# Kernel tuning notes

Measured on AMD Instinct MI355X. Metric: run time of the kernel, lower is better.

The kernel has to match this reference:

```python
import jax, jax.numpy as jnp
import numpy as np

N = 100000      # nodes per node type (asset, zone)
E = 1000000     # edges per edge type
HID = 64        # hidden_dim
HEADS = 2
CH = HID // HEADS  # 32, GATConv out_channels per head
L = 2           # num_layers
A = 64          # action_count
NG = 6          # global features
FW = 2 * HID + NG  # 134 feature width for heads


def _gat(xs_in, xd_in, W, a_src, a_dst, bias, src, dst, n_dst):
    """PyG GATConv (v1, add_self_loops=False, concat=True) for one edge type.
    xs_in: [Ns, HID] source feats, xd_in: [Nd, HID] dest feats (same lin weight W).
    Returns [n_dst, HEADS*CH]."""
    xs = (xs_in @ W).reshape(-1, HEADS, CH)
    xd = (xd_in @ W).reshape(-1, HEADS, CH)
    al_s = jnp.einsum('nhc,hc->nh', xs, a_src)
    al_d = jnp.einsum('nhc,hc->nh', xd, a_dst)
    al = jax.nn.leaky_relu(al_s[src] + al_d[dst], 0.2)       # [E, H]
    mx = jax.ops.segment_max(al, dst, num_segments=n_dst)    # segment softmax (stable)
    mx = jnp.where(jnp.isfinite(mx), mx, 0.0)                # empty segments
    ex = jnp.exp(al - mx[dst])
    den = jax.ops.segment_sum(ex, dst, num_segments=n_dst)
    w = ex / (den[dst] + 1e-16)                              # PyG softmax eps
    msg = xs[src] * w[:, :, None]                            # [E, H, C]
    out = jax.ops.segment_sum(msg.reshape(msg.shape[0], HEADS * CH), dst, num_segments=n_dst)
    return out + bias


def setup_inputs() -> dict:
    key = jax.random.key(0)
    ks = jax.random.split(key, 24)
    s = 0.05
    inp = {
        'x_asset': jax.random.normal(ks[0], (N, 16), jnp.float32),
        'x_zone': jax.random.normal(ks[1], (N, 32), jnp.float32),
        'ei_zz': jax.random.randint(ks[2], (2, E), 0, N, dtype=jnp.int32),
        'ei_az': jax.random.randint(ks[3], (2, E), 0, N, dtype=jnp.int32),
        'ei_za': jax.random.randint(ks[4], (2, E), 0, N, dtype=jnp.int32),
        'gvec': jax.random.uniform(ks[5], (NG,), jnp.float32),
        'mask': jax.random.randint(ks[6], (A,), 0, 2) == 1,
        'proj_W_asset': jax.random.normal(ks[7], (16, HID), jnp.float32) * s,
        'proj_b_asset': jnp.zeros((HID,), jnp.float32),
        'proj_W_zone': jax.random.normal(ks[8], (32, HID), jnp.float32) * s,
        'proj_b_zone': jnp.zeros((HID,), jnp.float32),
        'gat_W': jax.random.normal(ks[9], (L, 3, HID, HID), jnp.float32) * s,
        'gat_asrc': jax.random.normal(ks[10], (L, 3, HEADS, CH), jnp.float32) * s,
        'gat_adst': jax.random.normal(ks[11], (L, 3, HEADS, CH), jnp.float32) * s,
        'gat_bias': jnp.zeros((L, 3, HID), jnp.float32),
        'actor_W1': jax.random.normal(ks[12], (FW, HID), jnp.float32) * s,
        'actor_b1': jnp.zeros((HID,), jnp.float32),
        'actor_W2': jax.random.normal(ks[13], (HID, A), jnp.float32) * s,
        'actor_b2': jnp.zeros((A,), jnp.float32),
        'critic_W1': jax.random.normal(ks[14], (FW, HID), jnp.float32) * s,
        'critic_b1': jnp.zeros((HID,), jnp.float32),
        'critic_W2': jax.random.normal(ks[15], (HID, 1), jnp.float32) * s,
        'critic_b2': jnp.zeros((1,), jnp.float32),
    }
    return inp


def reference(x_asset, x_zone, ei_zz, ei_az, ei_za, gvec, mask,
              proj_W_asset, proj_b_asset, proj_W_zone, proj_b_zone,
              gat_W, gat_asrc, gat_adst, gat_bias,
              actor_W1, actor_b1, actor_W2, actor_b2,
              critic_W1, critic_b1, critic_W2, critic_b2):
    # input projections per node type
    ha = x_asset @ proj_W_asset + proj_b_asset   # [N, HID]
    hz = x_zone @ proj_W_zone + proj_b_zone      # [N, HID]
    # HeteroConv stack: edge types 0=(zone,near,zone) 1=(asset,in,zone) 2=(zone,contains,asset), aggr='sum'
    for l in range(L):
        z_zz = _gat(hz, hz, gat_W[l, 0], gat_asrc[l, 0], gat_adst[l, 0], gat_bias[l, 0], ei_zz[0], ei_zz[1], N)
        z_az = _gat(ha, hz, gat_W[l, 1], gat_asrc[l, 1], gat_adst[l, 1], gat_bias[l, 1], ei_az[0], ei_az[1], N)
        a_za = _gat(hz, ha, gat_W[l, 2], gat_asrc[l, 2], gat_adst[l, 2], gat_bias[l, 2], ei_za[0], ei_za[1], N)
        hz = jax.nn.relu(z_zz + z_az)
        ha = jax.nn.relu(a_za)
    # mean pool per node type, sorted order: asset, zone
    pooled = jnp.concatenate([ha.mean(axis=0), hz.mean(axis=0)])
    feats = jnp.concatenate([pooled, gvec])      # [FW]
    logits = jax.nn.relu(feats @ actor_W1 + actor_b1) @ actor_W2 + actor_b2   # [A]
    value = jax.nn.relu(feats @ critic_W1 + critic_b1) @ critic_W2 + critic_b2  # [1]
    m = jnp.where(mask.any(), mask, jnp.ones_like(mask))
    masked = jnp.where(m, logits, -jnp.inf)
    return jnp.concatenate([masked, value])      # [A+1]: masked logits + value
```

## Files before the change

kernel.cpp:

```cpp
#include <hip/hip_runtime.h>
#include <math.h>

#define CE 8192
#define BSH 9
#define BMAXB 512
#define ASTR 104
#define DSTR 72

typedef __attribute__((ext_vector_type(8))) short bf16x8;
typedef __attribute__((ext_vector_type(4))) float f32x4;
typedef __attribute__((ext_vector_type(2))) float f32x2;

__device__ __forceinline__ unsigned short f2bf(float f) {
    unsigned u = __float_as_uint(f);
    u += 0x7fffu + ((u >> 16) & 1u);
    return (unsigned short)(u >> 16);
}
__device__ __forceinline__ float bf2f(unsigned short u) {
    return __uint_as_float(((unsigned)u) << 16);
}

__global__ __launch_bounds__(256) void gemm2_k(const float* __restrict__ Xa,
                                               const float* __restrict__ Xz,
                                               const float* __restrict__ Wa,
                                               const float* __restrict__ Wz,
                                               const float* __restrict__ ba,
                                               const float* __restrict__ bz,
                                               unsigned short* __restrict__ outa,
                                               unsigned short* __restrict__ outz,
                                               int n) {
    const int y = blockIdx.y;
    const float* X = y ? Xz : Xa;
    const float* W = y ? Wz : Wa;
    const float* bias = y ? bz : ba;
    unsigned short* outb = y ? outz : outa;
    const int kshift = y ? 5 : 4;
    const int K = 1 << kshift;

    __shared__ float sXt[64 * 68];
    __shared__ float sW[64 * 64];
    __shared__ float sB[64];
    const int tid = threadIdx.x;
    const int row0 = blockIdx.x * 64;

    for (int i = tid * 4; i < 64 * K; i += 1024) {
        int r = i >> kshift, k = i & (K - 1);
        int row = row0 + r;
        float4 v = make_float4(0.f, 0.f, 0.f, 0.f);
        if (row < n) v = *(const float4*)(X + (size_t)row * K + k);
        sXt[(k + 0) * 68 + r] = v.x;
        sXt[(k + 1) * 68 + r] = v.y;
        sXt[(k + 2) * 68 + r] = v.z;
        sXt[(k + 3) * 68 + r] = v.w;
    }
    for (int i = tid * 4; i < K * 64; i += 1024)
        *(float4*)(sW + i) = *(const float4*)(W + i);
    if (tid < 64) sB[tid] = bias[tid];
    __syncthreads();

    const int tc = tid & 15, tr = tid >> 4;
    float acc[4][4] = {};
#pragma unroll 8
    for (int k = 0; k < K; ++k) {
        float4 a = *(const float4*)(sXt + k * 68 + tr * 4);
        float4 b = *(const float4*)(sW + k * 64 + tc * 4);
        acc[0][0] += a.x * b.x; acc[0][1] += a.x * b.y; acc[0][2] += a.x * b.z; acc[0][3] += a.x * b.w;
        acc[1][0] += a.y * b.x; acc[1][1] += a.y * b.y; acc[1][2] += a.y * b.z; acc[1][3] += a.y * b.w;
        acc[2][0] += a.z * b.x; acc[2][1] += a.z * b.y; acc[2][2] += a.z * b.z; acc[2][3] += a.z * b.w;
        acc[3][0] += a.w * b.x; acc[3][1] += a.w * b.y; acc[3][2] += a.w * b.z; acc[3][3] += a.w * b.w;
    }
#pragma unroll
    for (int i = 0; i < 4; ++i) {
        int row = row0 + tr * 4 + i;
        if (row < n) {
            float4 o;
            o.x = acc[i][0] + sB[tc * 4 + 0];
            o.y = acc[i][1] + sB[tc * 4 + 1];
            o.z = acc[i][2] + sB[tc * 4 + 2];
            o.w = acc[i][3] + sB[tc * 4 + 3];
            ushort4 v4 = make_ushort4(f2bf(o.x), f2bf(o.y), f2bf(o.z), f2bf(o.w));
            *(ushort4*)(outb + (size_t)row * 64 + tc * 4) = v4;
        }
    }
}

__global__ void prep_k(const float* __restrict__ gW, const float* __restrict__ gad,
                       unsigned short* __restrict__ Wbt, float* __restrict__ Wd3All) {
    int b = blockIdx.x;
    int t = threadIdx.x;
    if (b < 6) {
        for (int i = t; i < 4096; i += 384) {
            int nn = i >> 6, k = i & 63;
            Wbt[(size_t)b * 4096 + i] = f2bf(gW[(size_t)b * 4096 + k * 64 + nn]);
        }
    } else {
        int l = b - 6;
        int et = t >> 7, r = t & 127;
        int k = r >> 1, h = r & 1;
        const float* W = gW + (size_t)l * 3 * 4096 + et * 4096;
        const float* adst = gad + (size_t)l * 3 * 64 + et * 64;
        float s = 0.f;
        for (int c = 0; c < 32; ++c) s += W[k * 64 + h * 32 + c] * adst[h * 32 + c];
        Wd3All[l * 384 + t] = s;
    }
}

__global__ __launch_bounds__(256) void gemm_mfma3_k(const unsigned short* __restrict__ hzb,
                                                    const unsigned short* __restrict__ hab,
                                                    const unsigned short* __restrict__ WbtL,
                                                    const float* __restrict__ gasL,
                                                    const float* __restrict__ Wd3,
                                                    unsigned char* __restrict__ ts0,
                                                    unsigned char* __restrict__ ts1,
                                                    unsigned char* __restrict__ ts2,
                                                    float2* __restrict__ als0,
                                                    float2* __restrict__ als1,
                                                    float2* __restrict__ als2,
                                                    float2* __restrict__ ald_zz,
                                                    float2* __restrict__ ald_az,
                                                    float2* __restrict__ ald_za, int n) {
    const int et = blockIdx.y;
    const unsigned short* Xb = (et == 1) ? hab : hzb;
    const unsigned short* Wt = WbtL + (size_t)et * 4096;
    const float* asrc = gasL + et * 64;
    unsigned char* ts8 = (et == 0) ? ts0 : (et == 1) ? ts1 : ts2;
    float2* alsOut = (et == 0) ? als0 : (et == 1) ? als1 : als2;

    __shared__ unsigned short sA[64 * ASTR];
    __shared__ unsigned short sB[64 * ASTR];
    __shared__ float sAs[64];
    __shared__ float sWd[384];
    const int tid = threadIdx.x;
    const int row0 = blockIdx.x * 64;

    for (int i = tid; i < 512; i += 256) {
        int r = i >> 3, seg = i & 7;
        int row = row0 + r;
        uint4 v = make_uint4(0, 0, 0, 0);
        if (row < n) v = *(const uint4*)(Xb + (size_t)row * 64 + seg * 8);
        *(uint4*)(sA + r * ASTR + seg * 8) = v;
    }
    for (int i = tid; i < 512; i += 256) {
        int nn = i >> 3, seg = i & 7;
        *(uint4*)(sB + nn * ASTR + seg * 8) = *(const uint4*)(Wt + nn * 64 + seg * 8);
    }
    if (tid < 64) sAs[tid] = asrc[tid];
    for (int i = tid; i < 384; i += 256) sWd[i] = Wd3[i];
    __syncthreads();

    const int lane = tid & 63;
    const int w = tid >> 6;
    const int m = lane & 15, q = lane >> 4;

    bf16x8 a0 = *(const bf16x8*)(sA + (w * 16 + m) * ASTR + q * 8);
    bf16x8 a1 = *(const bf16x8*)(sA + (w * 16 + m) * ASTR + 32 + q * 8);
    f32x4 acc[4];
#pragma unroll
    for (int c = 0; c < 4; ++c) {
        bf16x8 b0 = *(const bf16x8*)(sB + (c * 16 + m) * ASTR + q * 8);
        bf16x8 b1 = *(const bf16x8*)(sB + (c * 16 + m) * ASTR + 32 + q * 8);
        f32x4 z = {0.f, 0.f, 0.f, 0.f};
        z = __builtin_amdgcn_mfma_f32_16x16x32_bf16(a0, b0, z, 0, 0, 0);
        z = __builtin_amdgcn_mfma_f32_16x16x32_bf16(a1, b1, z, 0, 0, 0);
        acc[c] = z;
    }
    float s0[4], s1[4];
#pragma unroll
    for (int r = 0; r < 4; ++r) {
        s0[r] = acc[0][r] * sAs[m] + acc[1][r] * sAs[16 + m];
        s1[r] = acc[2][r] * sAs[32 + m] + acc[3][r] * sAs[48 + m];
    }
#pragma unroll
    for (int off = 1; off < 16; off <<= 1) {
#pragma unroll
        for (int r = 0; r < 4; ++r) { s0[r] += __shfl_xor(s0[r], off); s1[r] += __shfl_xor(s1[r], off); }
    }
    if (m < 4) {
        int row = row0 + w * 16 + q * 4 + m;
        if (row < n) alsOut[row] = make_float2(s0[m], s1[m]);
    }

    if (et != 2) {
        const int rid = tid >> 2, part = tid & 3;
        const int row = row0 + rid;
        const unsigned short* rp = sA + rid * ASTR + part * 16;
        bf16x8 x0 = *(const bf16x8*)rp;
        bf16x8 x1 = *(const bf16x8*)(rp + 8);
        float xv[16];
#pragma unroll
        for (int i = 0; i < 8; ++i) {
            xv[i]     = bf2f((unsigned short)x0[i]);
            xv[8 + i] = bf2f((unsigned short)x1[i]);
        }
        const float* wd = sWd + (et == 0 ? 0 : 256);
        float p0 = 0.f, p1 = 0.f, t0 = 0.f, t1 = 0.f;
#pragma unroll
        for (int i = 0; i < 16; ++i) {
            int k = part * 16 + i;
            p0 += xv[i] * wd[2 * k];
            p1 += xv[i] * wd[2 * k + 1];
        }
        if (et == 0) {
#pragma unroll
            for (int i = 0; i < 16; ++i) {
                int k = part * 16 + i;
                t0 += xv[i] * sWd[128 + 2 * k];
                t1 += xv[i] * sWd[128 + 2 * k + 1];
            }
        }
        p0 += __shfl_xor(p0, 1); p0 += __shfl_xor(p0, 2);
        p1 += __shfl_xor(p1, 1); p1 += __shfl_xor(p1, 2);
        t0 += __shfl_xor(t0, 1); t0 += __shfl_xor(t0, 2);
        t1 += __shfl_xor(t1, 1); t1 += __shfl_xor(t1, 2);
        if (part == 0 && row < n) {
            if (et == 0) {
                ald_zz[row] = make_float2(p0, p1);
                ald_az[row] = make_float2(t0, t1);
            } else {
                ald_za[row] = make_float2(p0, p1);
            }
        }
    }

    __syncthreads();
    unsigned char* sD = (unsigned char*)sA;
#pragma unroll
    for (int c = 0; c < 4; ++c) {
        int pk01 = __builtin_amdgcn_cvt_pk_fp8_f32(acc[c][0], acc[c][1], 0, false);
        int pk23 = __builtin_amdgcn_cvt_pk_fp8_f32(acc[c][2], acc[c][3], 0, false);
        int rb = w * 16 + q * 4;
        int col = c * 16 + m;
        sD[(rb + 0) * DSTR + col] = (unsigned char)(pk01 & 0xff);
        sD[(rb + 1) * DSTR + col] = (unsigned char)((pk01 >> 8) & 0xff);
        sD[(rb + 2) * DSTR + col] = (unsigned char)(pk23 & 0xff);
        sD[(rb + 3) * DSTR + col] = (unsigned char)((pk23 >> 8) & 0xff);
    }
    __syncthreads();
    for (int i = tid; i < 512; i += 256) {
        int r = i >> 3, seg = i & 7;
        int row = row0 + r;
        if (row < n)
            *(uint2*)(ts8 + (size_t)row * 64 + seg * 8) = *(const uint2*)(sD + r * DSTR + seg * 8);
    }
}

__global__ __launch_bounds__(1024) void chunk_hist_k(const int* __restrict__ e0p,
                                                     const int* __restrict__ e1p,
                                                     const int* __restrict__ e2p,
                                                     int* __restrict__ cnt,
                                                     int E, int CB, int NBr) {
    int b = blockIdx.x;
    int et = b / CB, c = b - et * CB;
    const int* dst = (et == 0 ? e0p : et == 1 ? e1p : e2p) + E;
    __shared__ int lcnt[BMAXB];
    int t = threadIdx.x;
    for (int i = t; i < NBr; i += 1024) lcnt[i] = 0;
    __syncthreads();
    int base = c * CE;
    for (int i = t; i < CE; i += 1024) {
        int e = base + i;
        if (e < E) atomicAdd(&lcnt[dst[e] >> BSH], 1);
    }
    __syncthreads();
    int rowbase = et * NBr;
    for (int i = t; i < NBr; i += 1024) cnt[(size_t)(rowbase + i) * CB + c] = lcnt[i];
}
__global__ __launch_bounds__(256) void row_scan_k(int* __restrict__ cnt,
                                                  int* __restrict__ btot, int CB) {
    size_t row = (size_t)blockIdx.x * CB;
    __shared__ int buf[512];
    int t = threadIdx.x;
    int o0 = (t < CB) ? cnt[row + t] : 0;
    int o1 = (t + 256 < CB) ? cnt[row + t + 256] : 0;
    buf[t] = o0; buf[t + 256] = o1;
    __syncthreads();
    for (int off = 1; off < 512; off <<= 1) {
        int v0 = (t >= off) ? buf[t - off] : 0;
        int v1 = (t + 256 >= off) ? buf[t + 256 - off] : 0;
        __syncthreads();
        buf[t] += v0; buf[t + 256] += v1;
        __syncthreads();
    }
    if (t < CB) cnt[row + t] = buf[t] - o0;
    if (t + 256 < CB) cnt[row + t + 256] = buf[t + 256] - o1;
    if (t == 0) btot[blockIdx.x] = buf[511];
}
__global__ __launch_bounds__(1024) void btot_scan_k(const int* __restrict__ btot,
                                                    int* __restrict__ bbase,
                                                    int* __restrict__ bOff,
                                                    int NT, int E,
                                                    int* __restrict__ rowptrAll, int N) {
    __shared__ int buf[1024];
    int t = threadIdx.x;
    int v = (t < NT) ? btot[t] : 0;
    buf[t] = v;
    __syncthreads();
    for (int off = 1; off < 1024; off <<= 1) {
        int u = (t >= off) ? buf[t - off] : 0;
        __syncthreads();
        buf[t] += u;
        __syncthreads();
    }
    if (t < NT) { int e = buf[t] - v; bbase[t] = e; bOff[t] = e; }
    if (t == 0) {
        bOff[NT] = 3 * E;
        rowptrAll[N] = E;
        rowptrAll[(N + 1) + N] = 2 * E;
        rowptrAll[2 * (N + 1) + N] = 3 * E;
    }
}
__global__ __launch_bounds__(1024) void chunk_scatter_k(const int* __restrict__ e0p,
                                                        const int* __restrict__ e1p,
                                                        const int* __restrict__ e2p,
                                                        const int* __restrict__ cnt,
                                                        const int* __restrict__ bbase,
                                                        int* __restrict__ pairs,
                                                        int E, int CB, int NBr) {
    int b = blockIdx.x;
    int et = b / CB, c = b - et * CB;
    const int* eb = (et == 0 ? e0p : et == 1 ? e1p : e2p);
    __shared__ int lcur[BMAXB];
    int t = threadIdx.x;
    int rb = et * NBr;
    for (int i = t; i < NBr; i += 1024) lcur[i] = bbase[rb + i] + cnt[(size_t)(rb + i) * CB + c];
    __syncthreads();
    int base = c * CE;
    for (int i = t; i < CE; i += 1024) {
        int e = base + i;
        if (e < E) {
            int d = eb[E + e];
            int pos = atomicAdd(&lcur[d >> BSH], 1);
            pairs[pos] = ((d & (BMAXB - 1)) << 20) | eb[e];
        }
    }
}
__global__ __launch_bounds__(512) void bucket_local_k(const int* __restrict__ pairs,
                                                      const int* __restrict__ bOff,
                                                      int* __restrict__ rowptrAll,
                                                      int* __restrict__ ssrc, int N, int NBr) {
    int b = blockIdx.x;
    int et = b / NBr, lb = b - et * NBr;
    int beg = bOff[b], end = bOff[b + 1];
    int node0 = lb << BSH;
    int* rowptr = rowptrAll + (size_t)et * (N + 1);
    __shared__ int deg[512];
    __shared__ int cur[512];
    __shared__ int wsum[8];
    int t = threadIdx.x, lane = t & 63, wq = t >> 6;
    deg[t] = 0;
    __syncthreads();
    for (int j = beg + t; j < end; j += 512)
        atomicAdd(&deg[pairs[j] >> 20], 1);
    __syncthreads();
    int v = deg[t];
    int x = v;
#pragma unroll
    for (int off = 1; off < 64; off <<= 1) {
        int u = __shfl_up(x, off);
        if (lane >= off) x += u;
    }
    if (lane == 63) wsum[wq] = x;
    __syncthreads();
    int basep = 0;
#pragma unroll
    for (int q = 0; q < 8; ++q) basep += (q < wq) ? wsum[q] : 0;
    int e0 = beg + basep + x - v;
    cur[t] = e0;
    int n0 = node0 + t;
    if (n0 < N) rowptr[n0] = e0;
    __syncthreads();
    for (int j = beg + t; j < end; j += 512) {
        int p = pairs[j];
        int pos = atomicAdd(&cur[p >> 20], 1);
        ssrc[pos] = p & 0xFFFFF;
    }
}

__global__ __launch_bounds__(256) void gat_out2_k(const int* __restrict__ rowptr0,
                                                  const int* __restrict__ rowptr1,
                                                  const int* __restrict__ rowptr2,
                                                  const int* __restrict__ ssrc,
                                                  const float2* __restrict__ als0,
                                                  const float2* __restrict__ ald0,
                                                  const unsigned char* __restrict__ ts0,
                                                  const float2* __restrict__ als1,
                                                  const float2* __restrict__ ald1,
                                                  const unsigned char* __restrict__ ts1,
                                                  const float2* __restrict__ als2,
                                                  const float2* __restrict__ ald2,
                                                  const unsigned char* __restrict__ ts2,
                                                  const float* __restrict__ gbL,
                                                  unsigned short* __restrict__ outHz,
                                                  unsigned short* __restrict__ outHa,
                                                  int n) {
    const int y = blockIdx.y;
    const int nseg = y ? 1 : 2;
    int lane = threadIdx.x & 63;
    int gl = lane & 15;
    int wid = blockIdx.x * 16 + (threadIdx.x >> 4);
    if (wid >= n) return;
    const int r = gl >> 3;
    const int c0 = (gl & 7) * 8;
    const int gbase = lane & 48;

    float acc8[8] = {};
    for (int seg = 0; seg < nseg; ++seg) {
        const int* rowptr;
        const float2 *als, *ald;
        const unsigned char* ts8;
        if (y) { rowptr = rowptr2; als = als2; ald = ald2; ts8 = ts2; }
        else if (seg == 0) { rowptr = rowptr0; als = als0; ald = ald0; ts8 = ts0; }
        else { rowptr = rowptr1; als = als1; ald = ald1; ts8 = ts1; }
        int beg = rowptr[wid], end = rowptr[wid + 1];
        if (beg == end) continue;
        float2 bd = ald[wid];
        float d0 = 0.f, d1 = 0.f;
        float a8[8] = {};
        for (int cbeg = beg; cbeg < end; cbeg += 16) {
            int j = cbeg + gl;
            int s = 0; float e0 = 0.f, e1 = 0.f;
            if (j < end) {
                s = ssrc[j];
                float2 a = als[s];
                float l0 = a.x + bd.x; l0 = l0 > 0.f ? l0 : 0.2f * l0;
                float l1 = a.y + bd.y; l1 = l1 > 0.f ? l1 : 0.2f * l1;
                e0 = __expf(l0); e1 = __expf(l1);
            }
            d0 += e0; d1 += e1;
            int cnt = min(16, end - cbeg);
            uint2 rr[8]; float wv[8];
#pragma unroll
            for (int k = 0; k < 8; ++k) {
                int jj = 2 * k;
                if (jj < cnt) {
                    int srcLane = gbase + jj + r;
                    int sj = __shfl(s, srcLane);
                    float w0 = __shfl(e0, srcLane), w1 = __shfl(e1, srcLane);
                    float w = (c0 < 32) ? w0 : w1;
                    bool live = (jj + r) < cnt;
                    wv[k] = live ? w : 0.f;
                    if (live) rr[k] = *(const uint2*)(ts8 + (size_t)sj * 64 + c0);
                    else rr[k] = make_uint2(0, 0);
                } else { wv[k] = 0.f; rr[k] = make_uint2(0, 0); }
            }
#pragma unroll
            for (int k = 0; k < 8; ++k) {
                float w = wv[k];
                if (w != 0.f) {
                    f32x2 p0 = __builtin_amdgcn_cvt_pk_f32_fp8(rr[k].x, false);
                    f32x2 p1 = __builtin_amdgcn_cvt_pk_f32_fp8(rr[k].x, true);
                    f32x2 p2 = __builtin_amdgcn_cvt_pk_f32_fp8(rr[k].y, false);
                    f32x2 p3 = __builtin_amdgcn_cvt_pk_f32_fp8(rr[k].y, true);
                    a8[0] += p0.x * w; a8[1] += p0.y * w;
                    a8[2] += p1.x * w; a8[3] += p1.y * w;
                    a8[4] += p2.x * w; a8[5] += p2.y * w;
                    a8[6] += p3.x * w; a8[7] += p3.y * w;
                }
            }
        }
#pragma unroll
        for (int off = 1; off < 16; off <<= 1) { d0 += __shfl_xor(d0, off); d1 += __shfl_xor(d1, off); }
#pragma unroll
        for (int i = 0; i < 8; ++i) a8[i] += __shfl_xor(a8[i], 8);
        float inv = (c0 < 32) ? 1.f / (d0 + 1e-16f) : 1.f / (d1 + 1e-16f);
#pragma unroll
        for (int i = 0; i < 8; ++i) acc8[i] += a8[i] * inv;
    }

    if (r == 0) {
        const float* biasA = y ? gbL + 128 : gbL;
        const float* biasB = y ? nullptr : gbL + 64;
        float4 bA1 = *(const float4*)(biasA + c0);
        float4 bA2 = *(const float4*)(biasA + c0 + 4);
        float b8[8] = { bA1.x, bA1.y, bA1.z, bA1.w, bA2.x, bA2.y, bA2.z, bA2.w };
        if (biasB) {
            float4 bB1 = *(const float4*)(biasB + c0);
            float4 bB2 = *(const float4*)(biasB + c0 + 4);
            b8[0] += bB1.x; b8[1] += bB1.y; b8[2] += bB1.z; b8[3] += bB1.w;
            b8[4] += bB2.x; b8[5] += bB2.y; b8[6] += bB2.z; b8[7] += bB2.w;
        }
        float v8[8];
#pragma unroll
        for (int i = 0; i < 8; ++i) v8[i] = fmaxf(acc8[i] + b8[i], 0.f);
        unsigned short* outBf = y ? outHa : outHz;
        unsigned short* bp = outBf + (size_t)wid * 64 + c0;
        ushort4 u1 = make_ushort4(f2bf(v8[0]), f2bf(v8[1]), f2bf(v8[2]), f2bf(v8[3]));
        ushort4 u2 = make_ushort4(f2bf(v8[4]), f2bf(v8[5]), f2bf(v8[6]), f2bf(v8[7]));
        *(ushort4*)bp = u1;
        *(ushort4*)(bp + 4) = u2;
    }
}

__global__ __launch_bounds__(256) void pool_k(const unsigned short* __restrict__ hab,
                                              const unsigned short* __restrict__ hzb,
                                              float* __restrict__ sums, int n) {
    __shared__ float red[2][16][64];
    int tid = threadIdx.x;
    int c4 = (tid & 15) * 4;
    int rq = tid >> 4;
    float la[4] = {}, lz[4] = {};
    for (int row = blockIdx.x * 16 + rq; row < n; row += gridDim.x * 16) {
        ushort4 va = *(const ushort4*)(hab + (size_t)row * 64 + c4);
        ushort4 vz = *(const ushort4*)(hzb + (size_t)row * 64 + c4);
        la[0] += bf2f(va.x); la[1] += bf2f(va.y); la[2] += bf2f(va.z); la[3] += bf2f(va.w);
        lz[0] += bf2f(vz.x); lz[1] += bf2f(vz.y); lz[2] += bf2f(vz.z); lz[3] += bf2f(vz.w);
    }
#pragma unroll
    for (int i = 0; i < 4; ++i) { red[0][rq][c4 + i] = la[i]; red[1][rq][c4 + i] = lz[i]; }
    __syncthreads();
    if (tid < 64) {
        float ta = 0.f, tz = 0.f;
#pragma unroll
        for (int rr = 0; rr < 16; ++rr) { ta += red[0][rr][tid]; tz += red[1][rr][tid]; }
        atomicAdd(sums + tid, ta);
        atomicAdd(sums + 64 + tid, tz);
    }
}

__global__ __launch_bounds__(64) void head_k(const float* __restrict__ sums,
                                             const float* __restrict__ gvec,
                                             const unsigned char* __restrict__ mask,
                                             const float* __restrict__ aW1, const float* __restrict__ ab1,
                                             const float* __restrict__ aW2, const float* __restrict__ ab2,
                                             const float* __restrict__ cW1, const float* __restrict__ cb1,
                                             const float* __restrict__ cW2, const float* __restrict__ cb2,
                                             float* __restrict__ out, float invn) {
    __shared__ float f[134];
    __shared__ float h1a[64];
    int t = threadIdx.x;
    f[t] = sums[t] * invn;
    f[64 + t] = sums[64 + t] * invn;
    if (t < 6) f[128 + t] = gvec[t];
    __syncthreads();
    float a = ab1[t], c = cb1[t];
    for (int i = 0; i < 134; ++i) {
        float fv = f[i];
        a += fv * aW1[i * 64 + t];
        c += fv * cW1[i * 64 + t];
    }
    h1a[t] = fmaxf(a, 0.f);
    float vp = fmaxf(c, 0.f) * cW2[t];
    __syncthreads();
    float lg = ab2[t];
    for (int j = 0; j < 64; ++j) lg += h1a[j] * aW2[j * 64 + t];
    for (int off = 32; off; off >>= 1) vp += __shfl_down(vp, off);
    unsigned char mb = mask[t];
    unsigned long long bal = __ballot(mb != 0);
    float ov = (bal == 0ull || mb) ? lg : -3.0e38f;
    out[t] = ov;
    if (t == 0) out[64] = vp + cb2[0];
}

extern "C" void kernel_launch(void* const* d_in, const int* in_sizes, int n_in,
                              void* d_out, int out_size, void* d_ws, size_t ws_size,
                              hipStream_t stream) {
    const float* x_asset = (const float*)d_in[0];
    const float* x_zone  = (const float*)d_in[1];
    const int* ei[3] = { (const int*)d_in[2], (const int*)d_in[3], (const int*)d_in[4] };
    const float* gvec = (const float*)d_in[5];
    const unsigned char* mask = (const unsigned char*)d_in[6];
    const float* pWa = (const float*)d_in[7];
    const float* pba = (const float*)d_in[8];
    const float* pWz = (const float*)d_in[9];
    const float* pbz = (const float*)d_in[10];
    const float* gW  = (const float*)d_in[11];
    const float* gas = (const float*)d_in[12];
    const float* gad = (const float*)d_in[13];
    const float* gb  = (const float*)d_in[14];
    const float* aW1 = (const float*)d_in[15];
    const float* ab1 = (const float*)d_in[16];
    const float* aW2 = (const float*)d_in[17];
    const float* ab2 = (const float*)d_in[18];
    const float* cW1 = (const float*)d_in[19];
    const float* cb1 = (const float*)d_in[20];
    const float* cW2 = (const float*)d_in[21];
    const float* cb2 = (const float*)d_in[22];

    const int N = in_sizes[0] / 16;
    const int E = in_sizes[2] / 2;
    const int NBr = (N + 511) >> BSH;
    const int CB  = (E + CE - 1) / CE;
    const int NT  = 3 * NBr;

    float* ws = (float*)d_ws;
    size_t off = 0;
    unsigned short* hab = (unsigned short*)(ws + off); off += (size_t)N * 32;
    unsigned short* hzb = (unsigned short*)(ws + off); off += (size_t)N * 32;
    unsigned char* ts3[3];
    for (int et = 0; et < 3; ++et) { ts3[et] = (unsigned char*)(ws + off); off += (size_t)N * 16; }
    float2* als3[3];
    for (int et = 0; et < 3; ++et) { als3[et] = (float2*)(ws + off); off += (size_t)2 * N; }
    float2* ald3[3];
    for (int et = 0; et < 3; ++et) { ald3[et] = (float2*)(ws + off); off += (size_t)2 * N; }
    unsigned short* Wbt = (unsigned short*)(ws + off); off += 12288 + 64;
    float* Wd3All = ws + off; off += 768;
    float* sums = ws + off; off += 128;
    int* rowptrAll = (int*)(ws + off); off += (size_t)3 * (N + 1);
    int* ssrcAll   = (int*)(ws + off); off += (size_t)3 * E;
    int* pairs     = (int*)(ws + off); off += (size_t)3 * E;
    int* cnt   = (int*)(ws + off); off += (size_t)NT * CB;
    int* btot  = (int*)(ws + off); off += 1024;
    int* bbase = (int*)(ws + off); off += 1024;
    int* bOff  = (int*)(ws + off); off += (size_t)(NT + 1);

    const int gGemm = (N + 63) / 64;
    const int gGat  = (N + 15) / 16;

    chunk_hist_k<<<3 * CB, 1024, 0, stream>>>(ei[0], ei[1], ei[2], cnt, E, CB, NBr);
    row_scan_k<<<NT, 256, 0, stream>>>(cnt, btot, CB);
    btot_scan_k<<<1, 1024, 0, stream>>>(btot, bbase, bOff, NT, E, rowptrAll, N);
    chunk_scatter_k<<<3 * CB, 1024, 0, stream>>>(ei[0], ei[1], ei[2], cnt, bbase, pairs, E, CB, NBr);
    bucket_local_k<<<NT, 512, 0, stream>>>(pairs, bOff, rowptrAll, ssrcAll, N, NBr);

    prep_k<<<8, 384, 0, stream>>>(gW, gad, Wbt, Wd3All);
    gemm2_k<<<dim3(gGemm, 2), 256, 0, stream>>>(x_asset, x_zone, pWa, pWz, pba, pbz,
                                                hab, hzb, N);

    for (int l = 0; l < 2; ++l) {
        gemm_mfma3_k<<<dim3(gGemm, 3), 256, 0, stream>>>(hzb, hab,
                                                         Wbt + (size_t)l * 3 * 4096,
                                                         gas + (size_t)l * 3 * 64,
                                                         Wd3All + (size_t)l * 384,
                                                         ts3[0], ts3[1], ts3[2],
                                                         als3[0], als3[1], als3[2],
                                                         ald3[0], ald3[1], ald3[2], N);
        gat_out2_k<<<dim3(gGat, 2), 256, 0, stream>>>(rowptrAll, rowptrAll + (N + 1),
                                                      rowptrAll + 2 * (N + 1), ssrcAll,
                                                      als3[0], ald3[0], ts3[0],
                                                      als3[1], ald3[1], ts3[1],
                                                      als3[2], ald3[2], ts3[2],
                                                      gb + (size_t)l * 3 * 64,
                                                      hzb, hab, N);
    }

    hipMemsetAsync(sums, 0, 128 * sizeof(float), stream);
    pool_k<<<256, 256, 0, stream>>>(hab, hzb, sums, N);
    head_k<<<1, 64, 0, stream>>>(sums, gvec, mask,
                                 aW1, ab1, aW2, ab2, cW1, cb1, cW2, cb2,
                                 (float*)d_out, 1.0f / (float)N);
}
```

Measured before the change: 410.4 us.

## Stage scatter outputs in LDS for coalesced writes; pack fp8 stores via lane shuffles

Measured after the change: 378.7 us. 1.08x faster.

```diff
diff --git a/kernel.cpp b/kernel.cpp
--- a/kernel.cpp
+++ b/kernel.cpp
@@ -224,16 +224,22 @@
 
     __syncthreads();
     unsigned char* sD = (unsigned char*)sA;
+    const int s = m & 3;
+    const int rowx = ((s & 1) << 1) | (s >> 1);
+    const int colb = (m & ~3);
 #pragma unroll
     for (int c = 0; c < 4; ++c) {
         int pk01 = __builtin_amdgcn_cvt_pk_fp8_f32(acc[c][0], acc[c][1], 0, false);
         int pk23 = __builtin_amdgcn_cvt_pk_fp8_f32(acc[c][2], acc[c][3], 0, false);
+        unsigned D = ((unsigned)pk01 & 0xFFFFu) | ((unsigned)pk23 << 16);
+        unsigned P = (unsigned)__shfl_xor((int)D, 1);
+        unsigned A = (s & 1) ? __builtin_amdgcn_perm(D, P, 0x07030602u)
+                             : __builtin_amdgcn_perm(D, P, 0x01050004u);
+        unsigned Q = (unsigned)__shfl_xor((int)A, 2);
+        unsigned B = (s & 2) ? __builtin_amdgcn_perm(A, Q, 0x07060302u)
+                             : __builtin_amdgcn_perm(A, Q, 0x01000504u);
         int rb = w * 16 + q * 4;
-        int col = c * 16 + m;
-        sD[(rb + 0) * DSTR + col] = (unsigned char)(pk01 & 0xff);
-        sD[(rb + 1) * DSTR + col] = (unsigned char)((pk01 >> 8) & 0xff);
-        sD[(rb + 2) * DSTR + col] = (unsigned char)(pk23 & 0xff);
-        sD[(rb + 3) * DSTR + col] = (unsigned char)((pk23 >> 8) & 0xff);
+        *(unsigned*)(sD + (rb + rowx) * DSTR + c * 16 + colb) = B;
     }
     __syncthreads();
     for (int i = tid; i < 512; i += 256) {
@@ -319,20 +325,58 @@
     int b = blockIdx.x;
     int et = b / CB, c = b - et * CB;
     const int* eb = (et == 0 ? e0p : et == 1 ? e1p : e2p);
+    __shared__ int lhist[BMAXB];
     __shared__ int lcur[BMAXB];
+    __shared__ int wsum[16];
+    __shared__ int lbuf[CE];
+    __shared__ int tgt[CE];
     int t = threadIdx.x;
     int rb = et * NBr;
-    for (int i = t; i < NBr; i += 1024) lcur[i] = bbase[rb + i] + cnt[(size_t)(rb + i) * CB + c];
+    for (int i = t; i < NBr; i += 1024) lhist[i] = 0;
     __syncthreads();
     int base = c * CE;
-    for (int i = t; i < CE; i += 1024) {
-        int e = base + i;
-        if (e < E) {
-            int d = eb[E + e];
-            int pos = atomicAdd(&lcur[d >> BSH], 1);
-            pairs[pos] = ((d & (BMAXB - 1)) << 20) | eb[e];
-        }
-    }
+    int d[8], sv[8];
+#pragma unroll
+    for (int k = 0; k < 8; ++k) {
+        int e = base + t + k * 1024;
+        bool live = e < E;
+        d[k] = live ? eb[E + e] : -1;
+        sv[k] = live ? eb[e] : 0;
+        if (live) atomicAdd(&lhist[d[k] >> BSH], 1);
+    }
+    __syncthreads();
+    int v = (t < NBr) ? lhist[t] : 0;
+    int x = v;
+#pragma unroll
+    for (int off = 1; off < 64; off <<= 1) {
+        int u = __shfl_up(x, off);
+        if ((t & 63) >= off) x += u;
+    }
+    if ((t & 63) == 63) wsum[t >> 6] = x;
+    __syncthreads();
+    int basep = 0;
+#pragma unroll
+    for (int qq = 0; qq < 16; ++qq) basep += (qq < (t >> 6)) ? wsum[qq] : 0;
+    int myofs = basep + x - v;
+    __syncthreads();
+    if (t < NBr) {
+        lcur[t] = myofs;
+        lhist[t] = bbase[rb + t] + cnt[(size_t)(rb + t) * CB + c] - myofs;
+    }
+    __syncthreads();
+#pragma unroll
+    for (int k = 0; k < 8; ++k) {
+        if (d[k] >= 0) {
+            int bkt = d[k] >> BSH;
+            int pos = atomicAdd(&lcur[bkt], 1);
+            lbuf[pos] = ((d[k] & (BMAXB - 1)) << 20) | sv[k];
+            tgt[pos] = lhist[bkt];
+        }
+    }
+    __syncthreads();
+    int tot = min(CE, E - base);
+    for (int p = t; p < tot; p += 1024)
+        pairs[tgt[p] + p] = lbuf[p];
 }
 __global__ __launch_bounds__(512) void bucket_local_k(const int* __restrict__ pairs,
                                                       const int* __restrict__ bOff,
@@ -346,6 +390,7 @@
     __shared__ int deg[512];
     __shared__ int cur[512];
     __shared__ int wsum[8];
+    __shared__ int lbuf[8192];
     int t = threadIdx.x, lane = t & 63, wq = t >> 6;
     deg[t] = 0;
     __syncthreads();
@@ -364,15 +409,28 @@
     int basep = 0;
 #pragma unroll
     for (int q = 0; q < 8; ++q) basep += (q < wq) ? wsum[q] : 0;
-    int e0 = beg + basep + x - v;
-    cur[t] = e0;
+    int localofs = basep + x - v;
+    int nedge = end - beg;
+    bool useLds = nedge <= 8192;
+    cur[t] = useLds ? localofs : beg + localofs;
     int n0 = node0 + t;
-    if (n0 < N) rowptr[n0] = e0;
-    __syncthreads();
-    for (int j = beg + t; j < end; j += 512) {
-        int p = pairs[j];
-        int pos = atomicAdd(&cur[p >> 20], 1);
-        ssrc[pos] = p & 0xFFFFF;
+    if (n0 < N) rowptr[n0] = beg + localofs;
+    __syncthreads();
+    if (useLds) {
+        for (int j = beg + t; j < end; j += 512) {
+            int p = pairs[j];
+            int pos = atomicAdd(&cur[p >> 20], 1);
+            lbuf[pos] = p & 0xFFFFF;
+        }
+        __syncthreads();
+        for (int p = t; p < nedge; p += 512)
+            ssrc[beg + p] = lbuf[p];
+    } else {
+        for (int j = beg + t; j < end; j += 512) {
+            int p = pairs[j];
+            int pos = atomicAdd(&cur[p >> 20], 1);
+            ssrc[pos] = p & 0xFFFFF;
+        }
     }
 }
 
```
